# Kernel tuning notes

Hardware: AMD Instinct MI355X
Metric: run time of the kernel (lower is better)

Reference implementation:

```python
import jax, jax.numpy as jnp
import numpy as np

N_NODES = 100000
N_GRAPHS = 512
NEG_SLOPE = 0.2
EPS = 1e-16


def gat_conv(x, W, a_src, a_dst, bias, src, dst, heads, out_ch, concat):
    # x: [N, Fin]; W: [Fin, heads*out_ch]; a_src/a_dst: [heads, out_ch]
    N = x.shape[0]
    h = (x @ W).reshape(N, heads, out_ch)                      # [N,H,C]
    alpha_src = jnp.einsum('nhc,hc->nh', h, a_src)             # [N,H]
    alpha_dst = jnp.einsum('nhc,hc->nh', h, a_dst)             # [N,H]
    e = alpha_src[src] + alpha_dst[dst]                        # [E,H]
    e = jnp.where(e > 0, e, NEG_SLOPE * e)                     # leaky relu
    # segment softmax over incoming edges per destination node
    m = jax.ops.segment_max(e, dst, num_segments=N)            # [N,H]
    m = jnp.where(jnp.isfinite(m), m, 0.0)
    ee = jnp.exp(e - m[dst])
    denom = jax.ops.segment_sum(ee, dst, num_segments=N)       # [N,H]
    alpha = ee / (denom[dst] + EPS)                            # [E,H]
    msg = h[src] * alpha[:, :, None]                           # [E,H,C]
    out = jax.ops.segment_sum(msg, dst, num_segments=N)        # [N,H,C]
    if concat:
        out = out.reshape(N, heads * out_ch)
    else:
        out = out.mean(axis=1)
    return out + bias


def setup_inputs() -> dict:
    key = jax.random.key(0)
    ks = jax.random.split(key, 12)
    x = jax.random.normal(ks[0], (N_NODES, 128), dtype=jnp.float32)
    edge_index = jax.random.randint(ks[1], (2, 1600000), 0, N_NODES, dtype=jnp.int64)
    batch = jnp.sort(jax.random.randint(ks[2], (N_NODES,), 0, N_GRAPHS, dtype=jnp.int64))
    s = 0.1
    W1 = jax.random.normal(ks[3], (128, 64), dtype=jnp.float32) * s
    a_src1 = jax.random.normal(ks[4], (8, 8), dtype=jnp.float32) * s
    a_dst1 = jax.random.normal(ks[5], (8, 8), dtype=jnp.float32) * s
    b1 = jnp.zeros((64,), dtype=jnp.float32)
    W2 = jax.random.normal(ks[6], (64, 10), dtype=jnp.float32) * s
    a_src2 = jax.random.normal(ks[7], (1, 10), dtype=jnp.float32) * s
    a_dst2 = jax.random.normal(ks[8], (1, 10), dtype=jnp.float32) * s
    b2 = jnp.zeros((10,), dtype=jnp.float32)
    return {"x": x, "edge_index": edge_index, "batch": batch,
            "W1": W1, "a_src1": a_src1, "a_dst1": a_dst1, "b1": b1,
            "W2": W2, "a_src2": a_src2, "a_dst2": a_dst2, "b2": b2}


def reference(x, edge_index, batch, W1, a_src1, a_dst1, b1, W2, a_src2, a_dst2, b2):
    N = x.shape[0]
    # PyG GATConv default add_self_loops=True
    loops = jnp.arange(N, dtype=edge_index.dtype)
    src = jnp.concatenate([edge_index[0], loops])
    dst = jnp.concatenate([edge_index[1], loops])
    # eval mode: dropout layers are identity
    h = gat_conv(x, W1, a_src1, a_dst1, b1, src, dst, heads=8, out_ch=8, concat=True)
    h = jax.nn.elu(h)
    h = gat_conv(h, W2, a_src2, a_dst2, b2, src, dst, heads=1, out_ch=10, concat=False)
    # global mean pool over graphs
    sums = jax.ops.segment_sum(h, batch, num_segments=N_GRAPHS)        # [G,10]
    cnts = jax.ops.segment_sum(jnp.ones((N, 1), h.dtype), batch, num_segments=N_GRAPHS)
    pooled = sums / jnp.maximum(cnts, 1.0)
    return jax.nn.log_softmax(pooled, axis=1)
```

## Files before the change

kernel.cpp:

```cpp
#include <hip/hip_runtime.h>
#include <math.h>

#define L2E 1.44269504088896f
#define LRELU(v) fmaxf((v), 0.2f * (v))

__device__ __forceinline__ float fexp2(float v) { return __builtin_amdgcn_exp2f(v); }

__device__ __forceinline__ unsigned short f2bf(float f) {
    unsigned u = __float_as_uint(f);
    u += 0x7FFFu + ((u >> 16) & 1u);
    return (unsigned short)(u >> 16);
}
__device__ __forceinline__ float bf2f(unsigned short b) {
    return __uint_as_float((unsigned)b << 16);
}

#define UPD4(mm, dd, AA, ev, GG)           \
    {                                      \
        float mn_ = fmaxf(mm, ev);         \
        float sc_ = fexp2(mm - mn_);       \
        float w_  = fexp2(ev - mn_);       \
        dd = dd * sc_ + w_;                \
        AA.x = AA.x * sc_ + w_ * (GG).x;   \
        AA.y = AA.y * sc_ + w_ * (GG).y;   \
        AA.z = AA.z * sc_ + w_ * (GG).z;   \
        AA.w = AA.w * sc_ + w_ * (GG).w;   \
        mm = mn_;                          \
    }
#define UPD1(mm, dd, aa, ev, hv)           \
    {                                      \
        float mn_ = fmaxf(mm, ev);         \
        float sc_ = fexp2(mm - mn_);       \
        float w_  = fexp2(ev - mn_);       \
        dd = dd * sc_ + w_;                \
        aa = aa * sc_ + w_ * (hv);         \
        mm = mn_;                          \
    }

#define CH 4096

__device__ __forceinline__ float4 b4f(ushort4 u) {
    float4 r;
    r.x = bf2f(u.x); r.y = bf2f(u.y); r.z = bf2f(u.z); r.w = bf2f(u.w);
    return r;
}

__global__ __launch_bounds__(256) void k_gemm1(
        const float* __restrict__ x, const float* __restrict__ W,
        const float* __restrict__ a_src, const float* __restrict__ a_dst,
        unsigned short* __restrict__ h1b, unsigned short* __restrict__ asrcb,
        float* __restrict__ adst, int N) {
    __shared__ float Wl[128 * 64];
    int tid = threadIdx.x;
    {
        const float4* W4 = (const float4*)W;
        float4* Wl4 = (float4*)Wl;
#pragma unroll
        for (int i = 0; i < 8; ++i) Wl4[tid + 256 * i] = W4[tid + 256 * i];
    }
    __syncthreads();

    int g = tid >> 3, h = tid & 7;
    int n0 = blockIdx.x * 256 + g * 8;
    const float4* x4 = (const float4*)x;

    float acc[8][8];
#pragma unroll
    for (int nn = 0; nn < 8; ++nn)
#pragma unroll
        for (int c = 0; c < 8; ++c) acc[nn][c] = 0.f;

    const float4 z4 = {0.f, 0.f, 0.f, 0.f};
    for (int kk = 0; kk < 32; ++kk) {
        float4 xa[8];
#pragma unroll
        for (int nn = 0; nn < 8; ++nn)
            xa[nn] = (n0 + nn < N) ? x4[(size_t)(n0 + nn) * 32 + kk] : z4;
#pragma unroll
        for (int j = 0; j < 4; ++j) {
            const float* wr = &Wl[(kk * 4 + j) * 64 + h * 8];
            float wv[8];
#pragma unroll
            for (int c = 0; c < 8; ++c) wv[c] = wr[c];
#pragma unroll
            for (int nn = 0; nn < 8; ++nn) {
                float xv = ((const float*)&xa[nn])[j];
#pragma unroll
                for (int c = 0; c < 8; ++c) acc[nn][c] = fmaf(xv, wv[c], acc[nn][c]);
            }
        }
    }

    const float* as = a_src + h * 8;
    const float* ad = a_dst + h * 8;
#pragma unroll
    for (int nn = 0; nn < 8; ++nn) {
        int n = n0 + nn;
        if (n >= N) break;
        float s = 0.f, d = 0.f;
        uint4 pk;
        unsigned* pw = (unsigned*)&pk;
#pragma unroll
        for (int c = 0; c < 8; c += 2) {
            s = fmaf(acc[nn][c], as[c], s);     d = fmaf(acc[nn][c], ad[c], d);
            s = fmaf(acc[nn][c+1], as[c+1], s); d = fmaf(acc[nn][c+1], ad[c+1], d);
            pw[c >> 1] = (unsigned)f2bf(acc[nn][c]) | ((unsigned)f2bf(acc[nn][c+1]) << 16);
        }
        *(uint4*)&h1b[(size_t)n * 64 + h * 8] = pk;
        asrcb[n * 8 + h] = f2bf(s * L2E);
        adst[n * 8 + h] = d * L2E;
    }
}


__global__ __launch_bounds__(256) void k_bhist(const int* __restrict__ dstE,
                                               const int* __restrict__ batch,
                                               int E, int NB, int G, int* __restrict__ bh) {
    __shared__ int lh[512];
    int tid = threadIdx.x, b = blockIdx.x;
    lh[tid] = 0; lh[tid + 256] = 0;
    __syncthreads();
#pragma unroll
    for (int i = 0; i < CH / 256; ++i) {
        int e = b * CH + i * 256 + tid;
        if (e < E) atomicAdd(&lh[batch[dstE[e]]], 1);
    }
    __syncthreads();
    if (tid < G)       bh[(size_t)tid * NB + b] = lh[tid];
    if (tid + 256 < G) bh[(size_t)(tid + 256) * NB + b] = lh[tid + 256];
}

__global__ __launch_bounds__(512) void k_mscan(const int* __restrict__ bh, int NB,
                                               int* __restrict__ pstart, int* __restrict__ total) {
    __shared__ int buf[512];
    int bin = blockIdx.x, t = threadIdx.x;
    int v = (t < NB) ? bh[(size_t)bin * NB + t] : 0;
    buf[t] = v;
    __syncthreads();
    for (int off = 1; off < 512; off <<= 1) {
        int u = (t >= off) ? buf[t - off] : 0;
        __syncthreads();
        buf[t] += u;
        __syncthreads();
    }
    if (t < NB) pstart[(size_t)bin * NB + t] = buf[t] - v;
    if (t == 511) total[bin] = buf[511];
}

__global__ __launch_bounds__(1024) void k_scan_top(const int* __restrict__ total, int nb,
                                                   int* __restrict__ boff) {
    __shared__ int buf[1024];
    int t = threadIdx.x;
    int v = (t < nb) ? total[t] : 0;
    buf[t] = v;
    __syncthreads();
    for (int off = 1; off < 1024; off <<= 1) {
        int u = (t >= off) ? buf[t - off] : 0;
        __syncthreads();
        buf[t] += u;
        __syncthreads();
    }
    if (t < nb) boff[t] = buf[t] - v;
}

__global__ __launch_bounds__(256) void k_bscatter(const int* __restrict__ srcE,
                                                  const int* __restrict__ dstE,
                                                  const int* __restrict__ batch,
                                                  const int* __restrict__ boff,
                                                  const int* __restrict__ pstart,
                                                  int E, int NB, int G, int2* __restrict__ pairs) {
    __shared__ int lstart[512];
    __shared__ int lc[512];
    int tid = threadIdx.x, b = blockIdx.x;
#pragma unroll
    for (int j = tid; j < 512; j += 256) {
        lstart[j] = (j < G) ? boff[j] + pstart[(size_t)j * NB + b] : 0;
        lc[j] = 0;
    }
    __syncthreads();
#pragma unroll
    for (int i = 0; i < CH / 256; ++i) {
        int e = b * CH + i * 256 + tid;
        if (e < E) {
            int s = srcE[e], d = dstE[e];
            int bin = batch[d];
            int old = atomicAdd(&lc[bin], 1);
            pairs[lstart[bin] + old] = make_int2(s, d);
        }
    }
}

__global__ __launch_bounds__(512) void k_csr_local(const int2* __restrict__ pairs,
                                                   const int* __restrict__ boff,
                                                   const int* __restrict__ batch,
                                                   int E, int N, int G,
                                                   int* __restrict__ cnt, int* __restrict__ excl,
                                                   int* __restrict__ srcs) {
    __shared__ int lcnt[512];
    __shared__ int buf[512];
    __shared__ int lcur[512];
    int g = blockIdx.x, t = threadIdx.x;
    int lo = 0, hi = N;
    while (lo < hi) { int mid = (lo + hi) >> 1; if (batch[mid] < g) lo = mid + 1; else hi = mid; }
    int ns = lo;
    hi = N;
    while (lo < hi) { int mid = (lo + hi) >> 1; if (batch[mid] < g + 1) lo = mid + 1; else hi = mid; }
    int ne = lo;
    int lnodes = ne - ns;
    int es = boff[g];
    int ee = (g + 1 < G) ? boff[g + 1] : E;

    lcnt[t] = 0;
    __syncthreads();
    for (int e = es + t; e < ee; e += 512) atomicAdd(&lcnt[pairs[e].y - ns], 1);
    __syncthreads();
    int v = lcnt[t];
    buf[t] = v;
    __syncthreads();
    for (int off = 1; off < 512; off <<= 1) {
        int u = (t >= off) ? buf[t - off] : 0;
        __syncthreads();
        buf[t] += u;
        __syncthreads();
    }
    int lex = buf[t] - v;
    lcur[t] = lex;
    if (t < lnodes) {
        cnt[ns + t] = v;
        excl[ns + t] = es + lex;
    }
    __syncthreads();
    for (int e = es + t; e < ee; e += 512) {
        int2 p = pairs[e];
        int pos = atomicAdd(&lcur[p.y - ns], 1);
        srcs[es + pos] = p.x;
    }
}

__global__ void k_gather1(const int* __restrict__ srcs, const int* __restrict__ excl,
                          const int* __restrict__ cnt,
                          const unsigned short* __restrict__ asrcb, const float* __restrict__ adst1,
                          const unsigned short* __restrict__ h1b, float* __restrict__ agg, int N) {
    int tid = blockIdx.x * 256 + threadIdx.x;
    int wave = tid >> 6;
    int lane = threadIdx.x & 63;
    int q = lane >> 4;
    int l = lane & 15;
    int wid = wave * 4 + q;
    if (wid >= N) return;
    int h = l >> 1;
    int c0 = l * 4;

    int beg = excl[wid];
    int cw  = cnt[wid];
    const int* sp = srcs + beg;
    float adh = adst1[wid * 8 + h];

    float4 A0 = b4f(*(const ushort4*)&h1b[(size_t)wid * 64 + c0]);
    float m0 = LRELU(bf2f(asrcb[wid * 8 + h]) + adh), d0 = 1.f;
    float4 A1 = {0.f, 0.f, 0.f, 0.f}, A2 = A1, A3 = A1;
    float m1 = -INFINITY, d1 = 0.f;
    float m2 = -INFINITY, d2 = 0.f;
    float m3 = -INFINITY, d3 = 0.f;

    int i = 0;
    for (; i + 4 <= cw; i += 4) {
        int s0 = sp[i], s1 = sp[i + 1], s2 = sp[i + 2], s3 = sp[i + 3];
        float e0 = LRELU(bf2f(asrcb[s0 * 8 + h]) + adh);
        float e1 = LRELU(bf2f(asrcb[s1 * 8 + h]) + adh);
        float e2 = LRELU(bf2f(asrcb[s2 * 8 + h]) + adh);
        float e3 = LRELU(bf2f(asrcb[s3 * 8 + h]) + adh);
        float4 g0 = b4f(*(const ushort4*)&h1b[(size_t)s0 * 64 + c0]);
        float4 g1 = b4f(*(const ushort4*)&h1b[(size_t)s1 * 64 + c0]);
        float4 g2 = b4f(*(const ushort4*)&h1b[(size_t)s2 * 64 + c0]);
        float4 g3 = b4f(*(const ushort4*)&h1b[(size_t)s3 * 64 + c0]);
        UPD4(m0, d0, A0, e0, g0);
        UPD4(m1, d1, A1, e1, g1);
        UPD4(m2, d2, A2, e2, g2);
        UPD4(m3, d3, A3, e3, g3);
    }
    for (; i < cw; ++i) {
        int s = sp[i];
        float ev = LRELU(bf2f(asrcb[s * 8 + h]) + adh);
        float4 gv = b4f(*(const ushort4*)&h1b[(size_t)s * 64 + c0]);
        UPD4(m0, d0, A0, ev, gv);
    }
    float mM = fmaxf(fmaxf(m0, m1), fmaxf(m2, m3));
    float w0 = fexp2(m0 - mM), w1 = fexp2(m1 - mM);
    float w2 = fexp2(m2 - mM), w3 = fexp2(m3 - mM);
    float den = d0 * w0 + d1 * w1 + d2 * w2 + d3 * w3;
    float inv = 1.f / (den + 1e-16f);
    float4 r;
    r.x = (A0.x * w0 + A1.x * w1 + A2.x * w2 + A3.x * w3) * inv;
    r.y = (A0.y * w0 + A1.y * w1 + A2.y * w2 + A3.y * w3) * inv;
    r.z = (A0.z * w0 + A1.z * w1 + A2.z * w2 + A3.z * w3) * inv;
    r.w = (A0.w * w0 + A1.w * w1 + A2.w * w2 + A3.w * w3) * inv;
    *(float4*)&agg[(size_t)wid * 64 + c0] = r;
}

__global__ void k_fin1(const float* __restrict__ agg, const float* __restrict__ b1,
                       const float* __restrict__ W2,
                       const float* __restrict__ a_src2, const float* __restrict__ a_dst2,
                       unsigned short* __restrict__ h2b, unsigned short* __restrict__ asrc2b,
                       float* __restrict__ adst2, int N) {
    int n = blockIdx.x * 256 + threadIdx.x;
    if (n >= N) return;
    float acc[10];
#pragma unroll
    for (int j = 0; j < 10; ++j) acc[j] = 0.f;
    const float* ar = agg + (size_t)n * 64;
#pragma unroll 8
    for (int k = 0; k < 64; ++k) {
        float r = ar[k] + b1[k];
        r = r > 0.f ? r : expm1f(r);
#pragma unroll
        for (int j = 0; j < 10; ++j) acc[j] = fmaf(r, W2[k * 10 + j], acc[j]);
    }
    float s = 0.f, d = 0.f;
    unsigned pw[5];
#pragma unroll
    for (int j = 0; j < 10; j += 2) {
        s = fmaf(acc[j], a_src2[j], s);     d = fmaf(acc[j], a_dst2[j], d);
        s = fmaf(acc[j+1], a_src2[j+1], s); d = fmaf(acc[j+1], a_dst2[j+1], d);
        pw[j >> 1] = (unsigned)f2bf(acc[j]) | ((unsigned)f2bf(acc[j+1]) << 16);
    }
    unsigned* hw = (unsigned*)&h2b[(size_t)n * 10];
#pragma unroll
    for (int j = 0; j < 5; ++j) hw[j] = pw[j];
    asrc2b[n] = f2bf(s * L2E);
    adst2[n] = d * L2E;
}

__global__ void k_gather2(const int* __restrict__ srcs, const int* __restrict__ excl,
                          const int* __restrict__ cnt,
                          const unsigned short* __restrict__ asrc2b, const float* __restrict__ adst2,
                          const unsigned short* __restrict__ h2b, float* __restrict__ agg2, int N) {
    int tid = blockIdx.x * 256 + threadIdx.x;
    int wave = tid >> 6;
    int lane = threadIdx.x & 63;
    int q = lane >> 4;
    int l = lane & 15;
    int wid = wave * 4 + q;
    if (wid >= N) return;

    int beg = excl[wid];
    int cw  = cnt[wid];
    const int* sp = srcs + beg;
    float adn = adst2[wid];
    bool ld = l < 10;

    float m0 = LRELU(bf2f(asrc2b[wid]) + adn), d0 = 1.f;
    float a0 = ld ? bf2f(h2b[(size_t)wid * 10 + l]) : 0.f;
    float m1 = -INFINITY, d1 = 0.f, a1 = 0.f;
    float m2 = -INFINITY, d2 = 0.f, a2 = 0.f;
    float m3 = -INFINITY, d3 = 0.f, a3 = 0.f;

    int i = 0;
    for (; i + 4 <= cw; i += 4) {
        int s0 = sp[i], s1 = sp[i + 1], s2 = sp[i + 2], s3 = sp[i + 3];
        float e0 = LRELU(bf2f(asrc2b[s0]) + adn);
        float e1 = LRELU(bf2f(asrc2b[s1]) + adn);
        float e2 = LRELU(bf2f(asrc2b[s2]) + adn);
        float e3 = LRELU(bf2f(asrc2b[s3]) + adn);
        float g0 = ld ? bf2f(h2b[(size_t)s0 * 10 + l]) : 0.f;
        float g1 = ld ? bf2f(h2b[(size_t)s1 * 10 + l]) : 0.f;
        float g2 = ld ? bf2f(h2b[(size_t)s2 * 10 + l]) : 0.f;
        float g3 = ld ? bf2f(h2b[(size_t)s3 * 10 + l]) : 0.f;
        UPD1(m0, d0, a0, e0, g0);
        UPD1(m1, d1, a1, e1, g1);
        UPD1(m2, d2, a2, e2, g2);
        UPD1(m3, d3, a3, e3, g3);
    }
    for (; i < cw; ++i) {
        int s = sp[i];
        float ev = LRELU(bf2f(asrc2b[s]) + adn);
        float gv = ld ? bf2f(h2b[(size_t)s * 10 + l]) : 0.f;
        UPD1(m0, d0, a0, ev, gv);
    }
    float mM = fmaxf(fmaxf(m0, m1), fmaxf(m2, m3));
    float w0 = fexp2(m0 - mM), w1 = fexp2(m1 - mM);
    float w2 = fexp2(m2 - mM), w3 = fexp2(m3 - mM);
    float den = d0 * w0 + d1 * w1 + d2 * w2 + d3 * w3;
    float acc = a0 * w0 + a1 * w1 + a2 * w2 + a3 * w3;
    if (ld) agg2[(size_t)wid * 10 + l] = acc / (den + 1e-16f);
}

__global__ void k_pool_final(const float* __restrict__ agg2, const float* __restrict__ b2,
                             const int* __restrict__ batch, float* __restrict__ out,
                             int N, int G) {
    int g = blockIdx.x;
    int lo = 0, hi = N;
    while (lo < hi) { int mid = (lo + hi) >> 1; if (batch[mid] < g) lo = mid + 1; else hi = mid; }
    int s = lo;
    lo = s; hi = N;
    while (lo < hi) { int mid = (lo + hi) >> 1; if (batch[mid] < g + 1) lo = mid + 1; else hi = mid; }
    int e = lo;
    int tid = threadIdx.x;
    float acc[10];
#pragma unroll
    for (int j = 0; j < 10; ++j) acc[j] = 0.f;
    for (int n = s + tid; n < e; n += 256) {
        const float* r = agg2 + (size_t)n * 10;
#pragma unroll
        for (int j = 0; j < 10; ++j) acc[j] += r[j];
    }
    __shared__ float red[256 * 10];
#pragma unroll
    for (int j = 0; j < 10; ++j) red[tid * 10 + j] = acc[j];
    __syncthreads();
    for (int st = 128; st > 0; st >>= 1) {
        if (tid < st)
#pragma unroll
            for (int j = 0; j < 10; ++j) red[tid * 10 + j] += red[(tid + st) * 10 + j];
        __syncthreads();
    }
    if (tid == 0) {
        int c = e - s;
        float v[10], m = -1e30f;
#pragma unroll
        for (int j = 0; j < 10; ++j) {
            v[j] = (c > 0) ? red[j] / (float)c + b2[j] : 0.f;
            m = fmaxf(m, v[j]);
        }
        float ssum = 0.f;
#pragma unroll
        for (int j = 0; j < 10; ++j) ssum += expf(v[j] - m);
        float ls = logf(ssum);
#pragma unroll
        for (int j = 0; j < 10; ++j) out[(size_t)g * 10 + j] = v[j] - m - ls;
    }
}

extern "C" void kernel_launch(void* const* d_in, const int* in_sizes, int n_in,
                              void* d_out, int out_size, void* d_ws, size_t ws_size,
                              hipStream_t stream) {
    const float* x     = (const float*)d_in[0];
    const int*   ei    = (const int*)d_in[1];
    const int*   batch = (const int*)d_in[2];
    const float* W1    = (const float*)d_in[3];
    const float* as1w  = (const float*)d_in[4];
    const float* ad1w  = (const float*)d_in[5];
    const float* b1    = (const float*)d_in[6];
    const float* W2    = (const float*)d_in[7];
    const float* as2w  = (const float*)d_in[8];
    const float* ad2w  = (const float*)d_in[9];
    const float* b2    = (const float*)d_in[10];

    const int N  = in_sizes[0] / 128;
    const int E  = in_sizes[1] / 2;
    const int G  = out_size / 10;
    const int* srcE = ei;
    const int* dstE = ei + E;

    auto cdiv = [](long long a, long long b) { return (int)((a + b - 1) / b); };
    const int NB = cdiv(E, CH);

    size_t Nz = (size_t)N;
    unsigned short* h1b = (unsigned short*)d_ws;
    float* agg2  = (float*)d_ws;
    unsigned short* asrc1b = h1b + Nz * 64;
    float* adst1 = (float*)(asrc1b + Nz * 8);
    unsigned short* h2b = (unsigned short*)(adst1 + Nz * 8);
    unsigned short* asrc2b = h2b + Nz * 10;
    float* adst2 = (float*)(asrc2b + Nz + (Nz & 1));
    float* agg1  = adst2 + Nz;
    int2*  pairs = (int2*)agg1;
    int* cntA    = (int*)(agg1 + Nz * 64);
    int* exclA   = cntA + Nz;
    int* srcsA   = exclA + Nz;
    int* bhA     = srcsA + E;
    int* pstartA = bhA + (size_t)512 * NB;
    int* totalA  = pstartA + (size_t)512 * NB;
    int* boffA   = totalA + 512;

    const int B = 256;

    k_gemm1<<<cdiv(N, 256), B, 0, stream>>>(x, W1, as1w, ad1w, h1b, asrc1b, adst1, N);

    k_bhist<<<NB, B, 0, stream>>>(dstE, batch, E, NB, G, bhA);
    k_mscan<<<512, 512, 0, stream>>>(bhA, NB, pstartA, totalA);
    k_scan_top<<<1, 1024, 0, stream>>>(totalA, G, boffA);
    k_bscatter<<<NB, B, 0, stream>>>(srcE, dstE, batch, boffA, pstartA, E, NB, G, pairs);
    k_csr_local<<<G, 512, 0, stream>>>(pairs, boffA, batch, E, N, G, cntA, exclA, srcsA);

    k_gather1<<<cdiv(N, 16), B, 0, stream>>>(srcsA, exclA, cntA, asrc1b, adst1, h1b, agg1, N);
    k_fin1<<<cdiv(N, B), B, 0, stream>>>(agg1, b1, W2, as2w, ad2w, h2b, asrc2b, adst2, N);

    k_gather2<<<cdiv(N, 16), B, 0, stream>>>(srcsA, exclA, cntA, asrc2b, adst2, h2b, agg2, N);

    k_pool_final<<<G, B, 0, stream>>>(agg2, b2, batch, (float*)d_out, N, G);
}
```

Baseline: 220.2 us.

## Restructure first-layer GEMM to stage x tile in LDS and read W via scalar loads

The first-layer projection kernel now loads a 64-node tile of x into padded, transposed shared memory with coalesced reads, instead of putting all of W in shared memory. Each wave computes 16 output columns for 64 nodes, reading W through wave-uniform addresses so the compiler can use scalar loads. This aims to fix the poorly coalesced per-thread float4 reads of x and the LDS pressure on W, at the cost of launching four times as many blocks and doing less register-level reuse per thread.

```diff
diff --git a/kernel.cpp b/kernel.cpp
--- a/kernel.cpp
+++ b/kernel.cpp
@@ -50,66 +50,60 @@
         const float* __restrict__ a_src, const float* __restrict__ a_dst,
         unsigned short* __restrict__ h1b, unsigned short* __restrict__ asrcb,
         float* __restrict__ adst, int N) {
-    __shared__ float Wl[128 * 64];
+    __shared__ float xl[128 * 65];
     int tid = threadIdx.x;
-    {
-        const float4* W4 = (const float4*)W;
-        float4* Wl4 = (float4*)Wl;
-#pragma unroll
-        for (int i = 0; i < 8; ++i) Wl4[tid + 256 * i] = W4[tid + 256 * i];
-    }
-    __syncthreads();
-
-    int g = tid >> 3, h = tid & 7;
-    int n0 = blockIdx.x * 256 + g * 8;
-    const float4* x4 = (const float4*)x;
-
-    float acc[8][8];
-#pragma unroll
-    for (int nn = 0; nn < 8; ++nn)
-#pragma unroll
-        for (int c = 0; c < 8; ++c) acc[nn][c] = 0.f;
-
-    const float4 z4 = {0.f, 0.f, 0.f, 0.f};
-    for (int kk = 0; kk < 32; ++kk) {
-        float4 xa[8];
-#pragma unroll
-        for (int nn = 0; nn < 8; ++nn)
-            xa[nn] = (n0 + nn < N) ? x4[(size_t)(n0 + nn) * 32 + kk] : z4;
-#pragma unroll
-        for (int j = 0; j < 4; ++j) {
-            const float* wr = &Wl[(kk * 4 + j) * 64 + h * 8];
-            float wv[8];
-#pragma unroll
-            for (int c = 0; c < 8; ++c) wv[c] = wr[c];
-#pragma unroll
-            for (int nn = 0; nn < 8; ++nn) {
-                float xv = ((const float*)&xa[nn])[j];
-#pragma unroll
-                for (int c = 0; c < 8; ++c) acc[nn][c] = fmaf(xv, wv[c], acc[nn][c]);
-            }
-        }
-    }
-
-    const float* as = a_src + h * 8;
-    const float* ad = a_dst + h * 8;
-#pragma unroll
-    for (int nn = 0; nn < 8; ++nn) {
-        int n = n0 + nn;
-        if (n >= N) break;
-        float s = 0.f, d = 0.f;
-        uint4 pk;
-        unsigned* pw = (unsigned*)&pk;
-#pragma unroll
-        for (int c = 0; c < 8; c += 2) {
-            s = fmaf(acc[nn][c], as[c], s);     d = fmaf(acc[nn][c], ad[c], d);
-            s = fmaf(acc[nn][c+1], as[c+1], s); d = fmaf(acc[nn][c+1], ad[c+1], d);
-            pw[c >> 1] = (unsigned)f2bf(acc[nn][c]) | ((unsigned)f2bf(acc[nn][c+1]) << 16);
-        }
-        *(uint4*)&h1b[(size_t)n * 64 + h * 8] = pk;
-        asrcb[n * 8 + h] = f2bf(s * L2E);
-        adst[n * 8 + h] = d * L2E;
-    }
+    int n0 = blockIdx.x * 64;
+    int nrem = N - n0;
+#pragma unroll
+    for (int i = 0; i < 32; ++i) {
+        int e = i * 256 + tid;
+        int row = e >> 7, k = e & 127;
+        float v = (row < nrem) ? x[(size_t)(n0 + row) * 128 + k] : 0.f;
+        xl[k * 65 + row] = v;
+    }
+    __syncthreads();
+
+    int wv = tid >> 6, lane = tid & 63;
+    int c0 = __builtin_amdgcn_readfirstlane(wv * 16);
+    const float* Wc = W + c0;
+
+    float acc[16];
+#pragma unroll
+    for (int c = 0; c < 16; ++c) acc[c] = 0.f;
+
+#pragma unroll 4
+    for (int k = 0; k < 128; ++k) {
+        float xv = xl[k * 65 + lane];
+#pragma unroll
+        for (int c = 0; c < 16; ++c)
+            acc[c] = fmaf(xv, Wc[k * 64 + c], acc[c]);
+    }
+
+    int n = n0 + lane;
+    if (n >= N) return;
+    int h0 = c0 >> 3;
+    float s0 = 0.f, d0 = 0.f, s1 = 0.f, d1 = 0.f;
+    uint4 pk0, pk1;
+    unsigned* p0 = (unsigned*)&pk0;
+    unsigned* p1 = (unsigned*)&pk1;
+#pragma unroll
+    for (int c = 0; c < 8; c += 2) {
+        s0 = fmaf(acc[c], a_src[c0 + c], s0);       d0 = fmaf(acc[c], a_dst[c0 + c], d0);
+        s0 = fmaf(acc[c+1], a_src[c0 + c + 1], s0); d0 = fmaf(acc[c+1], a_dst[c0 + c + 1], d0);
+        p0[c >> 1] = (unsigned)f2bf(acc[c]) | ((unsigned)f2bf(acc[c+1]) << 16);
+    }
+#pragma unroll
+    for (int c = 8; c < 16; c += 2) {
+        s1 = fmaf(acc[c], a_src[c0 + c], s1);       d1 = fmaf(acc[c], a_dst[c0 + c], d1);
+        s1 = fmaf(acc[c+1], a_src[c0 + c + 1], s1); d1 = fmaf(acc[c+1], a_dst[c0 + c + 1], d1);
+        p1[(c - 8) >> 1] = (unsigned)f2bf(acc[c]) | ((unsigned)f2bf(acc[c+1]) << 16);
+    }
+    *(uint4*)&h1b[(size_t)n * 64 + c0] = pk0;
+    *(uint4*)&h1b[(size_t)n * 64 + c0 + 8] = pk1;
+    asrcb[n * 8 + h0]     = f2bf(s0 * L2E);
+    asrcb[n * 8 + h0 + 1] = f2bf(s1 * L2E);
+    adst[n * 8 + h0]      = d0 * L2E;
+    adst[n * 8 + h0 + 1]  = d1 * L2E;
 }
 
 
@@ -475,7 +469,7 @@
 
     const int B = 256;
 
-    k_gemm1<<<cdiv(N, 256), B, 0, stream>>>(x, W1, as1w, ad1w, h1b, asrc1b, adst1, N);
+    k_gemm1<<<cdiv(N, 64), B, 0, stream>>>(x, W1, as1w, ad1w, h1b, asrc1b, adst1, N);
 
     k_bhist<<<NB, B, 0, stream>>>(dstE, batch, E, NB, G, bhA);
     k_mscan<<<512, 512, 0, stream>>>(bhA, NB, pstartA, totalA);
```

Measured after the change: 225.2 us. +2.2%, slower.

## Compute first-layer projection with bf16 MFMA and split attention logits into separate kernel

Applied to the files above, without the earlier changes.

The FP32 FMA tiled GEMM for x@W1 is replaced with a persistent kernel using 16x16x32 bf16 MFMA instructions. W is converted to bf16 fragments held in registers and x is converted on the fly. The per-head attention logit dot products move into a new k_alpha kernel that re-reads the bf16 h1 output. This trades an extra launch and an extra read of h1 for matrix-core throughput. The logits are now computed from bf16-rounded h and bf16 inputs, which lowers precision.

```diff
diff --git a/kernel.cpp b/kernel.cpp
--- a/kernel.cpp
+++ b/kernel.cpp
@@ -14,6 +14,9 @@
 __device__ __forceinline__ float bf2f(unsigned short b) {
     return __uint_as_float((unsigned)b << 16);
 }
+
+typedef __attribute__((ext_vector_type(8))) short bf16x8;
+typedef __attribute__((ext_vector_type(4))) float f32x4;
 
 #define UPD4(mm, dd, AA, ev, GG)           \
     {                                      \
@@ -45,71 +48,65 @@
     return r;
 }
 
-__global__ __launch_bounds__(256) void k_gemm1(
+__global__ __launch_bounds__(256) void k_gemm1_mfma(
         const float* __restrict__ x, const float* __restrict__ W,
-        const float* __restrict__ a_src, const float* __restrict__ a_dst,
-        unsigned short* __restrict__ h1b, unsigned short* __restrict__ asrcb,
-        float* __restrict__ adst, int N) {
-    __shared__ float Wl[128 * 64];
+        unsigned short* __restrict__ h1b, int N, int ntiles) {
     int tid = threadIdx.x;
-    {
-        const float4* W4 = (const float4*)W;
-        float4* Wl4 = (float4*)Wl;
-#pragma unroll
-        for (int i = 0; i < 8; ++i) Wl4[tid + 256 * i] = W4[tid + 256 * i];
-    }
-    __syncthreads();
-
-    int g = tid >> 3, h = tid & 7;
-    int n0 = blockIdx.x * 256 + g * 8;
-    const float4* x4 = (const float4*)x;
-
-    float acc[8][8];
-#pragma unroll
-    for (int nn = 0; nn < 8; ++nn)
-#pragma unroll
-        for (int c = 0; c < 8; ++c) acc[nn][c] = 0.f;
-
-    const float4 z4 = {0.f, 0.f, 0.f, 0.f};
-    for (int kk = 0; kk < 32; ++kk) {
-        float4 xa[8];
-#pragma unroll
-        for (int nn = 0; nn < 8; ++nn)
-            xa[nn] = (n0 + nn < N) ? x4[(size_t)(n0 + nn) * 32 + kk] : z4;
-#pragma unroll
-        for (int j = 0; j < 4; ++j) {
-            const float* wr = &Wl[(kk * 4 + j) * 64 + h * 8];
-            float wv[8];
-#pragma unroll
-            for (int c = 0; c < 8; ++c) wv[c] = wr[c];
-#pragma unroll
-            for (int nn = 0; nn < 8; ++nn) {
-                float xv = ((const float*)&xa[nn])[j];
-#pragma unroll
-                for (int c = 0; c < 8; ++c) acc[nn][c] = fmaf(xv, wv[c], acc[nn][c]);
-            }
+    int w = tid >> 6, l = tid & 63;
+    int c0 = w * 16;
+    int lr = l & 15;
+    int lg = l >> 4;
+
+    bf16x8 bfr[4];
+#pragma unroll
+    for (int kk = 0; kk < 4; ++kk)
+#pragma unroll
+        for (int j = 0; j < 8; ++j)
+            bfr[kk][j] = (short)f2bf(W[(size_t)(kk * 32 + lg * 8 + j) * 64 + c0 + lr]);
+
+    for (int t = blockIdx.x; t < ntiles; t += gridDim.x) {
+        int n0 = t * 16;
+        int n = n0 + lr;
+        const float4* xr = (const float4*)(x + (size_t)(n < N ? n : 0) * 128);
+        f32x4 acc = {0.f, 0.f, 0.f, 0.f};
+#pragma unroll
+        for (int kk = 0; kk < 4; ++kk) {
+            float4 u0 = xr[kk * 8 + lg * 2];
+            float4 u1 = xr[kk * 8 + lg * 2 + 1];
+            bf16x8 afr;
+            afr[0] = (short)f2bf(u0.x); afr[1] = (short)f2bf(u0.y);
+            afr[2] = (short)f2bf(u0.z); afr[3] = (short)f2bf(u0.w);
+            afr[4] = (short)f2bf(u1.x); afr[5] = (short)f2bf(u1.y);
+            afr[6] = (short)f2bf(u1.z); afr[7] = (short)f2bf(u1.w);
+            acc = __builtin_amdgcn_mfma_f32_16x16x32_bf16(afr, bfr[kk], acc, 0, 0, 0);
         }
-    }
-
+#pragma unroll
+        for (int r = 0; r < 4; ++r) {
+            int nn = n0 + lg * 4 + r;
+            if (nn < N) h1b[(size_t)nn * 64 + c0 + lr] = f2bf(acc[r]);
+        }
+    }
+}
+
+__global__ void k_alpha(const unsigned short* __restrict__ h1b,
+                        const float* __restrict__ a_src, const float* __restrict__ a_dst,
+                        unsigned short* __restrict__ asrcb, float* __restrict__ adst, int N) {
+    int t = blockIdx.x * 256 + threadIdx.x;
+    if (t >= N * 8) return;
+    int n = t >> 3, h = t & 7;
+    uint4 hw = *(const uint4*)&h1b[(size_t)n * 64 + h * 8];
+    const unsigned short* hu = (const unsigned short*)&hw;
     const float* as = a_src + h * 8;
     const float* ad = a_dst + h * 8;
-#pragma unroll
-    for (int nn = 0; nn < 8; ++nn) {
-        int n = n0 + nn;
-        if (n >= N) break;
-        float s = 0.f, d = 0.f;
-        uint4 pk;
-        unsigned* pw = (unsigned*)&pk;
-#pragma unroll
-        for (int c = 0; c < 8; c += 2) {
-            s = fmaf(acc[nn][c], as[c], s);     d = fmaf(acc[nn][c], ad[c], d);
-            s = fmaf(acc[nn][c+1], as[c+1], s); d = fmaf(acc[nn][c+1], ad[c+1], d);
-            pw[c >> 1] = (unsigned)f2bf(acc[nn][c]) | ((unsigned)f2bf(acc[nn][c+1]) << 16);
-        }
-        *(uint4*)&h1b[(size_t)n * 64 + h * 8] = pk;
-        asrcb[n * 8 + h] = f2bf(s * L2E);
-        adst[n * 8 + h] = d * L2E;
-    }
+    float s = 0.f, d = 0.f;
+#pragma unroll
+    for (int c = 0; c < 8; ++c) {
+        float hv = bf2f(hu[c]);
+        s = fmaf(hv, as[c], s);
+        d = fmaf(hv, ad[c], d);
+    }
+    asrcb[t] = f2bf(s * L2E);
+    adst[t] = d * L2E;
 }
 
 
@@ -475,7 +472,10 @@
 
     const int B = 256;
 
-    k_gemm1<<<cdiv(N, 256), B, 0, stream>>>(x, W1, as1w, ad1w, h1b, asrc1b, adst1, N);
+    int ntiles = cdiv(N, 16);
+    int gB = ntiles < 2048 ? ntiles : 2048;
+    k_gemm1_mfma<<<gB, B, 0, stream>>>(x, W1, h1b, N, ntiles);
+    k_alpha<<<cdiv((long long)N * 8, B), B, 0, stream>>>(h1b, as1w, ad1w, asrc1b, adst1, N);
 
     k_bhist<<<NB, B, 0, stream>>>(dstE, batch, E, NB, G, bhA);
     k_mscan<<<512, 512, 0, stream>>>(bhA, NB, pstartA, totalA);
```

Result: faster. 207.6 us (-5.8%).
